# Kernel optimization log

Measured on AMD Instinct MI355X. Metric: run time of the kernel, lower is better.

The kernel has to match this reference:

```python
import jax, jax.numpy as jnp
import numpy as np

B, H, W = 8192, 5, 5
DICT, SE, CC, E, NZ = 14, 32, 64, 256, 512
EPS = 1e-4


def _conv(x, w, b):
    # x: [B,C,H,W], w: [O,C,3,3] -> SAME padding, stride 1
    y = jax.lax.conv_general_dilated(x, w, (1, 1), 'SAME',
                                     dimension_numbers=('NCHW', 'OIHW', 'NCHW'))
    return y + b[None, :, None, None]


def _embed(idx, table, cw, cb):
    emb = table[idx]                                  # [B,H,W,SE]
    # nn.Embedding(max_norm=1): renorm looked-up rows to norm <= 1
    n = jnp.sqrt(jnp.sum(emb * emb, axis=-1, keepdims=True))
    emb = emb * jnp.minimum(1.0, 1.0 / (n + 1e-7))
    x = jnp.transpose(emb, (0, 3, 1, 2))              # [B,SE,H,W]
    return _conv(x, cw, cb)                           # [B,CC,H,W]


def _phi(x, w1, b1, w2, b2, lw, lb):
    x = jax.nn.relu(_conv(x, w1, b1))
    x = jax.nn.relu(_conv(x, w2, b2))
    x = x.reshape(x.shape[0], -1)                     # [B, 32*H*W]
    x = x @ lw.T + lb                                 # [B, E]
    return x / (jnp.sqrt(jnp.sum(x * x, axis=1, keepdims=True)) + EPS)


def setup_inputs() -> dict:
    key = jax.random.key(0)
    ks = jax.random.split(key, 20)
    g = lambda k, s, sc=0.05: (jax.random.normal(k, s, jnp.float32) * sc)
    return {
        's': jax.random.randint(ks[0], (B, H, W), 0, DICT, dtype=jnp.int32),
        's_prime': jax.random.randint(ks[1], (B, H, W), 0, DICT, dtype=jnp.int32),
        'embed_table': g(ks[2], (DICT, SE), 1.0),
        'conv_embed_w': g(ks[3], (CC, SE, 3, 3)),
        'conv_embed_b': g(ks[4], (CC,)),
        'phi1_conv1_w': g(ks[5], (16, CC, 3, 3)),
        'phi1_conv1_b': g(ks[6], (16,)),
        'phi1_conv2_w': g(ks[7], (32, 16, 3, 3)),
        'phi1_conv2_b': g(ks[8], (32,)),
        'phi1_lin_w': g(ks[9], (E, H * W * 32)),
        'phi1_lin_b': g(ks[10], (E,)),
        'phi2_conv1_w': g(ks[11], (16, CC, 3, 3)),
        'phi2_conv1_b': g(ks[12], (16,)),
        'phi2_conv2_w': g(ks[13], (32, 16, 3, 3)),
        'phi2_conv2_b': g(ks[14], (32,)),
        'phi2_lin_w': g(ks[15], (E, H * W * 32)),
        'phi2_lin_b': g(ks[16], (E,)),
        'z_vectors': g(ks[17], (NZ, E), 1.0),
        'scale': jnp.ones((1,), jnp.float32),
    }


def reference(s, s_prime, embed_table, conv_embed_w, conv_embed_b,
              phi1_conv1_w, phi1_conv1_b, phi1_conv2_w, phi1_conv2_b,
              phi1_lin_w, phi1_lin_b,
              phi2_conv1_w, phi2_conv1_b, phi2_conv2_w, phi2_conv2_b,
              phi2_lin_w, phi2_lin_b, z_vectors, scale):
    xs = _embed(s, embed_table, conv_embed_w, conv_embed_b)
    xsp = _embed(s_prime, embed_table, conv_embed_w, conv_embed_b)
    embed1 = _phi(xs, phi1_conv1_w, phi1_conv1_b, phi1_conv2_w, phi1_conv2_b,
                  phi1_lin_w, phi1_lin_b)                 # [B,E]
    embed2 = _phi(xsp - xs, phi2_conv1_w, phi2_conv1_b, phi2_conv2_w,
                  phi2_conv2_b, phi2_lin_w, phi2_lin_b)   # [B,E]
    # codebook: L2-normalize (eps=0), cosine argmax, gather
    zn = z_vectors / jnp.sqrt(jnp.sum(z_vectors * z_vectors, axis=1, keepdims=True))
    z_inds = jnp.argmax(embed2 @ zn.T, axis=1)            # [B]
    z_matrix = zn[z_inds]                                 # [B,E]
    gramm = embed1 @ z_matrix.T                           # [B,B]
    return jnp.exp(scale) * gramm
```

## Files before the change

kernel.cpp:

```cpp
#include <hip/hip_runtime.h>
#include <hip/hip_bf16.h>

#define NB    8192
#define DICT  14
#define SE    32
#define CC    64
#define EDIM  256
#define NZV   512
#define C1N   16
#define C2N   32
#define J400  400
#define K800  800

typedef __attribute__((ext_vector_type(8))) short bf16x8;
typedef __attribute__((ext_vector_type(4))) float f32x4;

__device__ __forceinline__ void split_hl(float x, unsigned short& h, unsigned short& l) {
    unsigned u = __float_as_uint(x);
    unsigned short hh = (unsigned short)(u >> 16);
    float hf = __uint_as_float((unsigned)hh << 16);
    float lof = x - hf;
    unsigned ul = __float_as_uint(lof);
    l = (unsigned short)((ul + 0x7FFFu + ((ul >> 16) & 1u)) >> 16);
    h = hh;
}

__global__ __launch_bounds__(64) void k_norm_embed(const float* __restrict__ tab,
                                                   float* __restrict__ tn) {
    int d = blockIdx.x, l = threadIdx.x;
    float v = (l < SE) ? tab[d * SE + l] : 0.f;
    float s = v * v;
    #pragma unroll
    for (int o = 32; o > 0; o >>= 1) s += __shfl_down(s, o, 64);
    s = __shfl(s, 0, 64);
    float sc = fminf(1.f, 1.f / (sqrtf(s) + 1e-7f));
    if (l < SE) tn[d * SE + l] = v * sc;
}

__global__ __launch_bounds__(256) void k_norm_z(const float* __restrict__ z,
                                                unsigned short* __restrict__ znh,
                                                unsigned short* __restrict__ znl) {
    __shared__ float red[4];
    int r = blockIdx.x, t = threadIdx.x;
    float v = z[r * EDIM + t];
    float s = v * v;
    #pragma unroll
    for (int o = 32; o > 0; o >>= 1) s += __shfl_down(s, o, 64);
    if ((t & 63) == 0) red[t >> 6] = s;
    __syncthreads();
    float tot = red[0] + red[1] + red[2] + red[3];
    float nv = v / sqrtf(tot);
    unsigned short h, l;
    split_hl(nv, h, l);
    znh[r * EDIM + t] = h;
    znl[r * EDIM + t] = l;
}

__global__ __launch_bounds__(256) void k_prep_w(const float* __restrict__ lwa,
                                                const float* __restrict__ lwb,
                                                unsigned short* __restrict__ wh,
                                                unsigned short* __restrict__ wl) {
    int i = blockIdx.x * 256 + threadIdx.x;
    const int tot = 2 * EDIM * K800;
    if (i >= tot) return;
    float v = (i < EDIM * K800) ? lwa[i] : lwb[i - EDIM * K800];
    unsigned short h, l;
    split_hl(v, h, l);
    wh[i] = h; wl[i] = l;
}

__global__ __launch_bounds__(256) void k_build_A(const float* __restrict__ we,
                                                 const float* __restrict__ tn,
                                                 float* __restrict__ A) {
    int i = blockIdx.x * 256 + threadIdx.x;
    if (i >= DICT * CC * 9) return;
    int f = i % 9, c1 = (i / 9) % CC, d = i / (9 * CC);
    float acc = 0.f;
    #pragma unroll
    for (int c0 = 0; c0 < SE; c0++) acc += we[(c1 * SE + c0) * 9 + f] * tn[d * SE + c0];
    A[i] = acc;
}

__global__ __launch_bounds__(256) void k_build_beff(const float* __restrict__ w1a,
                                                    const float* __restrict__ b1a,
                                                    const float* __restrict__ w1b,
                                                    const float* __restrict__ b1b,
                                                    const float* __restrict__ be,
                                                    float* __restrict__ beff) {
    int t = blockIdx.x;
    const float* w1 = t ? w1b : w1a;
    const float* b1 = t ? b1b : b1a;
    for (int j = threadIdx.x; j < J400; j += blockDim.x) {
        int o = j / 25, y = (j / 5) % 5, x = j % 5;
        float acc = b1[o];
        if (t == 0) {
            for (int ey = 0; ey < 3; ey++) {
                int py = y + ey - 1; if (py < 0 || py > 4) continue;
                for (int ex = 0; ex < 3; ex++) {
                    int px = x + ex - 1; if (px < 0 || px > 4) continue;
                    for (int c1 = 0; c1 < CC; c1++)
                        acc += w1[((o * CC + c1) * 3 + ey) * 3 + ex] * be[c1];
                }
            }
        }
        beff[t * J400 + j] = acc;
    }
}

__global__ __launch_bounds__(256) void k_build_T(const float* __restrict__ w1a,
                                                 const float* __restrict__ w1b,
                                                 const float* __restrict__ A,
                                                 float* __restrict__ T) {
    int t = blockIdx.y;
    int qd = blockIdx.x;
    int d = qd % DICT, q = qd / DICT;
    int qy = q / 5, qx = q % 5;
    const float* w1 = t ? w1b : w1a;
    __shared__ float w1s[C1N * CC * 9];
    __shared__ float As[CC * 9];
    for (int i = threadIdx.x; i < C1N * CC * 9; i += 256) w1s[i] = w1[i];
    for (int i = threadIdx.x; i < CC * 9; i += 256) As[i] = A[d * CC * 9 + i];
    __syncthreads();
    float* Tout = T + (((size_t)t * 25 + q) * DICT + d) * J400;
    for (int j = threadIdx.x; j < J400; j += 256) {
        int o = j / 25, y = (j / 5) % 5, x = j % 5;
        float acc = 0.f;
        int py0 = max(0, max(y - 1, qy - 1)), py1 = min(4, min(y + 1, qy + 1));
        int px0 = max(0, max(x - 1, qx - 1)), px1 = min(4, min(x + 1, qx + 1));
        for (int py = py0; py <= py1; py++)
            for (int px = px0; px <= px1; px++) {
                int ey = py - y + 1, ex = px - x + 1;
                int fy = qy - py + 1, fx = qx - px + 1;
                const float* wp = &w1s[(o * CC) * 9 + (ey * 3 + ex)];
                const float* ap = &As[fy * 3 + fx];
                float pa = 0.f;
                #pragma unroll 8
                for (int c1 = 0; c1 < CC; c1++) pa += wp[c1 * 9] * ap[c1 * 9];
                acc += pa;
            }
        Tout[j] = acc;
    }
}

__global__ __launch_bounds__(256) void k_stage1(const int* __restrict__ s,
                                                const int* __restrict__ sp,
                                                const float* __restrict__ T,
                                                const float* __restrict__ beff,
                                                float* __restrict__ a1f) {
    int phi = blockIdx.y;
    __shared__ int s_sh[32][25], sp_sh[32][25];
    __shared__ float a_sh[32][J400 + 1];
    int b0 = blockIdx.x * 32;
    for (int i = threadIdx.x; i < 32 * 25; i += 256) {
        int si = i / 25, q = i % 25;
        s_sh[si][q] = s[(b0 + si) * 25 + q];
        if (phi) sp_sh[si][q] = sp[(b0 + si) * 25 + q];
    }
    __syncthreads();
    const float* Tt = T + (size_t)phi * 25 * DICT * J400;
    const float* be = beff + phi * J400;
    if (phi == 0) {
        for (int task = threadIdx.x; task < 32 * J400; task += 256) {
            int j = task % J400, si = task / J400;
            float acc = be[j];
            #pragma unroll
            for (int q = 0; q < 25; q++)
                acc += Tt[(q * DICT + s_sh[si][q]) * J400 + j];
            a_sh[si][j] = fmaxf(acc, 0.f);
        }
    } else {
        for (int task = threadIdx.x; task < 32 * J400; task += 256) {
            int j = task % J400, si = task / J400;
            float acc = be[j];
            #pragma unroll
            for (int q = 0; q < 25; q++)
                acc += Tt[(q * DICT + sp_sh[si][q]) * J400 + j]
                     - Tt[(q * DICT + s_sh[si][q]) * J400 + j];
            a_sh[si][j] = fmaxf(acc, 0.f);
        }
    }
    __syncthreads();
    float* outp = a1f + (size_t)phi * J400 * NB;
    for (int i = threadIdx.x; i < 32 * J400; i += 256) {
        int bl = i % 32, j = i / 32;
        outp[(size_t)j * NB + b0 + bl] = a_sh[bl][j];
    }
}

__global__ __launch_bounds__(256) void k_conv2(const float* __restrict__ a1f,
                                               const float* __restrict__ w2a,
                                               const float* __restrict__ b2a,
                                               const float* __restrict__ w2b,
                                               const float* __restrict__ b2b,
                                               float* __restrict__ a2f) {
    int t = blockIdx.y;
    const float* w2  = t ? w2b : w2a;
    const float* b2  = t ? b2b : b2a;
    const float* in0 = a1f + (size_t)t * J400 * NB;
    float* out0      = a2f + (size_t)t * K800 * NB;
    int b  = blockIdx.x * 64 + (threadIdx.x & 63);
    int og = blockIdx.z * 4 + (threadIdx.x >> 6);
    for (int o2g = 0; o2g < 4; o2g++) {
        int o2 = og * 4 + o2g;
        float acc[25];
        float bias = b2[o2];
        #pragma unroll
        for (int p = 0; p < 25; p++) acc[p] = bias;
        for (int c1 = 0; c1 < C1N; c1++) {
            float in[25];
            #pragma unroll
            for (int p = 0; p < 25; p++) in[p] = in0[(size_t)(c1 * 25 + p) * NB + b];
            #pragma unroll
            for (int ky = 0; ky < 3; ky++)
            #pragma unroll
            for (int kx = 0; kx < 3; kx++) {
                float w = w2[((o2 * C1N + c1) * 3 + ky) * 3 + kx];
                #pragma unroll
                for (int y = 0; y < 5; y++) {
                    int iy = y + ky - 1; if (iy < 0 || iy > 4) continue;
                    #pragma unroll
                    for (int x = 0; x < 5; x++) {
                        int ix = x + kx - 1; if (ix < 0 || ix > 4) continue;
                        acc[y * 5 + x] += w * in[iy * 5 + ix];
                    }
                }
            }
        }
        #pragma unroll
        for (int p = 0; p < 25; p++)
            out0[(size_t)(o2 * 25 + p) * NB + b] = fmaxf(acc[p], 0.f);
    }
}

__global__ __launch_bounds__(256) void k_linear_mfma(const float* __restrict__ a2f,
        const unsigned short* __restrict__ wh, const unsigned short* __restrict__ wl,
        const float* __restrict__ lba, const float* __restrict__ lbb,
        unsigned short* __restrict__ eh, unsigned short* __restrict__ el) {
    int phi = blockIdx.y;
    const float* Am = a2f + (size_t)phi * K800 * NB;
    const unsigned short* Wh = wh + (size_t)phi * EDIM * K800;
    const unsigned short* Wl = wl + (size_t)phi * EDIM * K800;
    const float* bias = phi ? lbb : lba;
    int b0 = blockIdx.x * 32;
    int tid = threadIdx.x;
    int wv = tid >> 6, lane = tid & 63, li = lane & 15, quad = lane >> 4;
    int n0 = wv * 64;
    int sb = tid & 31, kc = (tid >> 5) * 4;
    __shared__ __align__(16) unsigned short AhS[32][40], AlS[32][40];
    __shared__ float red[32][4];
    f32x4 acc[2][4];
    f32x4 zz = {0.f, 0.f, 0.f, 0.f};
    #pragma unroll
    for (int i = 0; i < 2; i++)
        #pragma unroll
        for (int j = 0; j < 4; j++) acc[i][j] = zz;

    for (int k0 = 0; k0 < K800; k0 += 32) {
        float x0 = Am[(size_t)(k0 + kc + 0) * NB + b0 + sb];
        float x1 = Am[(size_t)(k0 + kc + 1) * NB + b0 + sb];
        float x2 = Am[(size_t)(k0 + kc + 2) * NB + b0 + sb];
        float x3 = Am[(size_t)(k0 + kc + 3) * NB + b0 + sb];
        __syncthreads();
        unsigned short h0, l0, h1, l1, h2, l2, h3, l3;
        split_hl(x0, h0, l0); split_hl(x1, h1, l1);
        split_hl(x2, h2, l2); split_hl(x3, h3, l3);
        *(ushort4*)&AhS[sb][kc] = make_ushort4(h0, h1, h2, h3);
        *(ushort4*)&AlS[sb][kc] = make_ushort4(l0, l1, l2, l3);
        __syncthreads();
        bf16x8 ah0 = *(const bf16x8*)&AhS[li][quad * 8];
        bf16x8 ah1 = *(const bf16x8*)&AhS[16 + li][quad * 8];
        bf16x8 al0 = *(const bf16x8*)&AlS[li][quad * 8];
        bf16x8 al1 = *(const bf16x8*)&AlS[16 + li][quad * 8];
        #pragma unroll
        for (int nt = 0; nt < 4; nt++) {
            size_t wo = (size_t)(n0 + nt * 16 + li) * K800 + k0 + quad * 8;
            bf16x8 bh = *(const bf16x8*)(Wh + wo);
            bf16x8 bl = *(const bf16x8*)(Wl + wo);
            acc[0][nt] = __builtin_amdgcn_mfma_f32_16x16x32_bf16(ah0, bh, acc[0][nt], 0, 0, 0);
            acc[0][nt] = __builtin_amdgcn_mfma_f32_16x16x32_bf16(ah0, bl, acc[0][nt], 0, 0, 0);
            acc[0][nt] = __builtin_amdgcn_mfma_f32_16x16x32_bf16(al0, bh, acc[0][nt], 0, 0, 0);
            acc[1][nt] = __builtin_amdgcn_mfma_f32_16x16x32_bf16(ah1, bh, acc[1][nt], 0, 0, 0);
            acc[1][nt] = __builtin_amdgcn_mfma_f32_16x16x32_bf16(ah1, bl, acc[1][nt], 0, 0, 0);
            acc[1][nt] = __builtin_amdgcn_mfma_f32_16x16x32_bf16(al1, bh, acc[1][nt], 0, 0, 0);
        }
    }
    float q[2][4];
    #pragma unroll
    for (int mt = 0; mt < 2; mt++)
        #pragma unroll
        for (int r = 0; r < 4; r++) q[mt][r] = 0.f;
    #pragma unroll
    for (int mt = 0; mt < 2; mt++)
        #pragma unroll
        for (int nt = 0; nt < 4; nt++) {
            float bsv = bias[n0 + nt * 16 + li];
            #pragma unroll
            for (int r = 0; r < 4; r++) {
                float v = acc[mt][nt][r] + bsv;
                acc[mt][nt][r] = v;
                q[mt][r] += v * v;
            }
        }
    #pragma unroll
    for (int off = 1; off < 16; off <<= 1) {
        #pragma unroll
        for (int mt = 0; mt < 2; mt++)
            #pragma unroll
            for (int r = 0; r < 4; r++)
                q[mt][r] += __shfl_xor(q[mt][r], off, 64);
    }
    if (li == 0) {
        #pragma unroll
        for (int mt = 0; mt < 2; mt++)
            #pragma unroll
            for (int r = 0; r < 4; r++)
                red[mt * 16 + quad * 4 + r][wv] = q[mt][r];
    }
    __syncthreads();
    #pragma unroll
    for (int mt = 0; mt < 2; mt++) {
        #pragma unroll
        for (int r = 0; r < 4; r++) {
            int row = mt * 16 + quad * 4 + r;
            float tot = red[row][0] + red[row][1] + red[row][2] + red[row][3];
            float inv = 1.f / (sqrtf(tot) + 1e-4f);
            size_t base = (size_t)(phi * NB + b0 + row) * EDIM;
            #pragma unroll
            for (int nt = 0; nt < 4; nt++) {
                float v = acc[mt][nt][r] * inv;
                unsigned short h, l;
                split_hl(v, h, l);
                eh[base + n0 + nt * 16 + li] = h;
                el[base + n0 + nt * 16 + li] = l;
            }
        }
    }
}

__global__ __launch_bounds__(256) void k_scores_mfma(const unsigned short* __restrict__ eh,
        const unsigned short* __restrict__ el,
        const unsigned short* __restrict__ znh, const unsigned short* __restrict__ znl,
        float* __restrict__ C) {
    int m0 = blockIdx.x * 64;
    int wv = threadIdx.x >> 6, lane = threadIdx.x & 63;
    int li = lane & 15, quad = lane >> 4;
    int n0 = blockIdx.y * 256 + wv * 64;
    f32x4 acc[4][4];
    f32x4 zz = {0.f, 0.f, 0.f, 0.f};
    #pragma unroll
    for (int i = 0; i < 4; i++)
        #pragma unroll
        for (int j = 0; j < 4; j++) acc[i][j] = zz;
    for (int k0 = 0; k0 < EDIM; k0 += 32) {
        bf16x8 ah[4], al[4];
        #pragma unroll
        for (int mt = 0; mt < 4; mt++) {
            size_t ao = (size_t)(m0 + mt * 16 + li) * EDIM + k0 + quad * 8;
            ah[mt] = *(const bf16x8*)(eh + ao);
            al[mt] = *(const bf16x8*)(el + ao);
        }
        #pragma unroll
        for (int nt = 0; nt < 4; nt++) {
            size_t bo = (size_t)(n0 + nt * 16 + li) * EDIM + k0 + quad * 8;
            bf16x8 bh = *(const bf16x8*)(znh + bo);
            bf16x8 bl = *(const bf16x8*)(znl + bo);
            #pragma unroll
            for (int mt = 0; mt < 4; mt++) {
                acc[mt][nt] = __builtin_amdgcn_mfma_f32_16x16x32_bf16(ah[mt], bh, acc[mt][nt], 0, 0, 0);
                acc[mt][nt] = __builtin_amdgcn_mfma_f32_16x16x32_bf16(ah[mt], bl, acc[mt][nt], 0, 0, 0);
                acc[mt][nt] = __builtin_amdgcn_mfma_f32_16x16x32_bf16(al[mt], bh, acc[mt][nt], 0, 0, 0);
            }
        }
    }
    #pragma unroll
    for (int mt = 0; mt < 4; mt++)
        #pragma unroll
        for (int nt = 0; nt < 4; nt++)
            #pragma unroll
            for (int r = 0; r < 4; r++)
                C[(size_t)(m0 + mt * 16 + quad * 4 + r) * NZV + n0 + nt * 16 + li] = acc[mt][nt][r];
}

__global__ __launch_bounds__(64) void k_argmax(const float* __restrict__ C,
                                               int* __restrict__ idx) {
    int b = blockIdx.x, l = threadIdx.x;
    const float* row = C + (size_t)(NB + b) * NZV;
    float best = -3.0e38f; int bi = 0;
    for (int n = l; n < NZV; n += 64) {
        float v = row[n];
        if (v > best) { best = v; bi = n; }
    }
    #pragma unroll
    for (int o = 32; o > 0; o >>= 1) {
        float ov = __shfl_down(best, o, 64);
        int   oi = __shfl_down(bi, o, 64);
        if (ov > best || (ov == best && oi < bi)) { best = ov; bi = oi; }
    }
    if (l == 0) idx[b] = bi;
}

__global__ __launch_bounds__(256) void k_out(const float* __restrict__ C,
                                             const int* __restrict__ idx,
                                             const float* __restrict__ scale,
                                             float* __restrict__ out) {
    __shared__ float g[8][NZV];
    __shared__ int   id[2048];
    int i0 = blockIdx.y * 8;
    int j0 = blockIdx.x * 2048;
    float esc = expf(scale[0]);
    for (int u = threadIdx.x; u < 2048; u += 256) id[u] = idx[j0 + u];
    for (int u = threadIdx.x; u < 8 * NZV; u += 256) {
        int r = u >> 9, c = u & 511;
        g[r][c] = C[(size_t)(i0 + r) * NZV + c];
    }
    __syncthreads();
    int jb = threadIdx.x * 8;
    int myid[8];
    #pragma unroll
    for (int u = 0; u < 8; u++) myid[u] = id[jb + u];
    #pragma unroll
    for (int r = 0; r < 8; r++) {
        float4 o0, o1;
        o0.x = esc * g[r][myid[0]]; o0.y = esc * g[r][myid[1]];
        o0.z = esc * g[r][myid[2]]; o0.w = esc * g[r][myid[3]];
        o1.x = esc * g[r][myid[4]]; o1.y = esc * g[r][myid[5]];
        o1.z = esc * g[r][myid[6]]; o1.w = esc * g[r][myid[7]];
        float4* dst = (float4*)(out + (size_t)(i0 + r) * NB + j0 + jb);
        dst[0] = o0; dst[1] = o1;
    }
}

extern "C" void kernel_launch(void* const* d_in, const int* in_sizes, int n_in,
                              void* d_out, int out_size, void* d_ws, size_t ws_size,
                              hipStream_t stream) {
    const int*   s     = (const int*)d_in[0];
    const int*   sp    = (const int*)d_in[1];
    const float* tab   = (const float*)d_in[2];
    const float* wE    = (const float*)d_in[3];
    const float* bE    = (const float*)d_in[4];
    const float* w1a   = (const float*)d_in[5];
    const float* b1a   = (const float*)d_in[6];
    const float* w2a   = (const float*)d_in[7];
    const float* b2a   = (const float*)d_in[8];
    const float* lwa   = (const float*)d_in[9];
    const float* lba   = (const float*)d_in[10];
    const float* w1b   = (const float*)d_in[11];
    const float* b1b   = (const float*)d_in[12];
    const float* w2b   = (const float*)d_in[13];
    const float* b2b   = (const float*)d_in[14];
    const float* lwb   = (const float*)d_in[15];
    const float* lbb   = (const float*)d_in[16];
    const float* zv    = (const float*)d_in[17];
    const float* scale = (const float*)d_in[18];

    float* out = (float*)d_out;
    float* wsf = (float*)d_ws;

    float* tn   = wsf;
    float* Aw   = wsf + 448;
    float* beff = wsf + 8512;
    int*   idx  = (int*)(wsf + 9312);
    float* T    = wsf + 17504;
    float* Cm   = wsf + 297504;
    unsigned short* znh = (unsigned short*)(wsf + 8686112);
    unsigned short* znl = (unsigned short*)(wsf + 8751648);
    unsigned short* wh  = (unsigned short*)(wsf + 8817184);
    unsigned short* wl  = (unsigned short*)(wsf + 9021984);
    unsigned short* eh  = (unsigned short*)(wsf + 9226784);
    unsigned short* el  = (unsigned short*)(wsf + 11323936);

    float* a1f = out;
    float* a2f = out + 6553600;

    k_norm_embed<<<DICT, 64, 0, stream>>>(tab, tn);
    k_norm_z<<<NZV, 256, 0, stream>>>(zv, znh, znl);
    k_prep_w<<<1600, 256, 0, stream>>>(lwa, lwb, wh, wl);
    k_build_A<<<32, 256, 0, stream>>>(wE, tn, Aw);
    k_build_beff<<<2, 256, 0, stream>>>(w1a, b1a, w1b, b1b, bE, beff);
    k_build_T<<<dim3(25 * DICT, 2), 256, 0, stream>>>(w1a, w1b, Aw, T);
    k_stage1<<<dim3(NB / 32, 2), 256, 0, stream>>>(s, sp, T, beff, a1f);
    k_conv2<<<dim3(NB / 64, 2, 2), 256, 0, stream>>>(a1f, w2a, b2a, w2b, b2b, a2f);
    k_linear_mfma<<<dim3(NB / 32, 2), 256, 0, stream>>>(a2f, wh, wl, lba, lbb, eh, el);
    k_scores_mfma<<<dim3(2 * NB / 64, NZV / 256), 256, 0, stream>>>(eh, el, znh, znl, Cm);
    k_argmax<<<NB, 64, 0, stream>>>(Cm, idx);
    k_out<<<dim3(NB / 2048, NB / 8), 256, 0, stream>>>(Cm, idx, scale, out);
}
```

Baseline: 609.9 us.

## Fuse stage1, conv2, linear, scores and argmax into one per-tile kernel

Merges the table-lookup first conv, second conv, split-bf16 MFMA linear layer, normalization, codebook scoring and argmax into a single kernel that keeps each 32-sample tile in LDS. The large a1/a2/embedding intermediates no longer round-trip through global memory. The small prep kernels are also merged to cut launches. The fused kernel uses about 78 KB of LDS, which limits occupancy, and the conv2 stage now runs per tile with syncs between output-channel chunks.

```diff
diff --git a/kernel.cpp b/kernel.cpp
--- a/kernel.cpp
+++ b/kernel.cpp
@@ -9,8 +9,6 @@
 #define NZV   512
 #define C1N   16
 #define C2N   32
-#define J400  400
-#define K800  800
 
 typedef __attribute__((ext_vector_type(8))) short bf16x8;
 typedef __attribute__((ext_vector_type(4))) float f32x4;
@@ -37,73 +35,69 @@
     if (l < SE) tn[d * SE + l] = v * sc;
 }
 
-__global__ __launch_bounds__(256) void k_norm_z(const float* __restrict__ z,
-                                                unsigned short* __restrict__ znh,
-                                                unsigned short* __restrict__ znl) {
-    __shared__ float red[4];
-    int r = blockIdx.x, t = threadIdx.x;
-    float v = z[r * EDIM + t];
-    float s = v * v;
-    #pragma unroll
-    for (int o = 32; o > 0; o >>= 1) s += __shfl_down(s, o, 64);
-    if ((t & 63) == 0) red[t >> 6] = s;
-    __syncthreads();
-    float tot = red[0] + red[1] + red[2] + red[3];
-    float nv = v / sqrtf(tot);
-    unsigned short h, l;
-    split_hl(nv, h, l);
-    znh[r * EDIM + t] = h;
-    znl[r * EDIM + t] = l;
-}
-
-__global__ __launch_bounds__(256) void k_prep_w(const float* __restrict__ lwa,
-                                                const float* __restrict__ lwb,
-                                                unsigned short* __restrict__ wh,
-                                                unsigned short* __restrict__ wl) {
-    int i = blockIdx.x * 256 + threadIdx.x;
-    const int tot = 2 * EDIM * K800;
-    if (i >= tot) return;
-    float v = (i < EDIM * K800) ? lwa[i] : lwb[i - EDIM * K800];
-    unsigned short h, l;
-    split_hl(v, h, l);
-    wh[i] = h; wl[i] = l;
-}
-
-__global__ __launch_bounds__(256) void k_build_A(const float* __restrict__ we,
-                                                 const float* __restrict__ tn,
-                                                 float* __restrict__ A) {
-    int i = blockIdx.x * 256 + threadIdx.x;
-    if (i >= DICT * CC * 9) return;
-    int f = i % 9, c1 = (i / 9) % CC, d = i / (9 * CC);
-    float acc = 0.f;
-    #pragma unroll
-    for (int c0 = 0; c0 < SE; c0++) acc += we[(c1 * SE + c0) * 9 + f] * tn[d * SE + c0];
-    A[i] = acc;
-}
-
-__global__ __launch_bounds__(256) void k_build_beff(const float* __restrict__ w1a,
-                                                    const float* __restrict__ b1a,
-                                                    const float* __restrict__ w1b,
-                                                    const float* __restrict__ b1b,
-                                                    const float* __restrict__ be,
-                                                    float* __restrict__ beff) {
-    int t = blockIdx.x;
-    const float* w1 = t ? w1b : w1a;
-    const float* b1 = t ? b1b : b1a;
-    for (int j = threadIdx.x; j < J400; j += blockDim.x) {
-        int o = j / 25, y = (j / 5) % 5, x = j % 5;
-        float acc = b1[o];
-        if (t == 0) {
-            for (int ey = 0; ey < 3; ey++) {
-                int py = y + ey - 1; if (py < 0 || py > 4) continue;
-                for (int ex = 0; ex < 3; ex++) {
-                    int px = x + ex - 1; if (px < 0 || px > 4) continue;
-                    for (int c1 = 0; c1 < CC; c1++)
-                        acc += w1[((o * CC + c1) * 3 + ey) * 3 + ex] * be[c1];
-                }
-            }
-        }
-        beff[t * J400 + j] = acc;
+__global__ __launch_bounds__(256) void k_prep_zw(const float* __restrict__ z,
+        const float* __restrict__ lwa, const float* __restrict__ lwb,
+        unsigned short* __restrict__ znh, unsigned short* __restrict__ znl,
+        unsigned short* __restrict__ wh, unsigned short* __restrict__ wl) {
+    int bid = blockIdx.x, t = threadIdx.x;
+    if (bid < NZV) {
+        __shared__ float red[4];
+        float v = z[bid * EDIM + t];
+        float s = v * v;
+        #pragma unroll
+        for (int o = 32; o > 0; o >>= 1) s += __shfl_down(s, o, 64);
+        if ((t & 63) == 0) red[t >> 6] = s;
+        __syncthreads();
+        float tot = red[0] + red[1] + red[2] + red[3];
+        float nv = v / sqrtf(tot);
+        unsigned short h, l;
+        split_hl(nv, h, l);
+        znh[bid * EDIM + t] = h;
+        znl[bid * EDIM + t] = l;
+    } else {
+        int i = (bid - NZV) * 256 + t;
+        if (i < 2 * EDIM * 800) {
+            float v = (i < EDIM * 800) ? lwa[i] : lwb[i - EDIM * 800];
+            unsigned short h, l;
+            split_hl(v, h, l);
+            wh[i] = h; wl[i] = l;
+        }
+    }
+}
+
+__global__ __launch_bounds__(256) void k_prep_ab(const float* __restrict__ we,
+        const float* __restrict__ tn,
+        const float* __restrict__ w1a, const float* __restrict__ b1a,
+        const float* __restrict__ w1b, const float* __restrict__ b1b,
+        const float* __restrict__ be,
+        float* __restrict__ A, float* __restrict__ beff) {
+    if (blockIdx.x < 32) {
+        int i = blockIdx.x * 256 + threadIdx.x;
+        if (i >= DICT * CC * 9) return;
+        int f = i % 9, c1 = (i / 9) % CC, d = i / (9 * CC);
+        float acc = 0.f;
+        #pragma unroll
+        for (int c0 = 0; c0 < SE; c0++) acc += we[(c1 * SE + c0) * 9 + f] * tn[d * SE + c0];
+        A[i] = acc;
+    } else {
+        int t = blockIdx.x - 32;
+        const float* w1 = t ? w1b : w1a;
+        const float* b1 = t ? b1b : b1a;
+        for (int j = threadIdx.x; j < 400; j += blockDim.x) {
+            int o = j / 25, y = (j / 5) % 5, x = j % 5;
+            float acc = b1[o];
+            if (t == 0) {
+                for (int ey = 0; ey < 3; ey++) {
+                    int py = y + ey - 1; if (py < 0 || py > 4) continue;
+                    for (int ex = 0; ex < 3; ex++) {
+                        int px = x + ex - 1; if (px < 0 || px > 4) continue;
+                        for (int c1 = 0; c1 < CC; c1++)
+                            acc += w1[((o * CC + c1) * 3 + ey) * 3 + ex] * be[c1];
+                    }
+                }
+            }
+            beff[t * 400 + j] = acc;
+        }
     }
 }
 
@@ -121,8 +115,8 @@
     for (int i = threadIdx.x; i < C1N * CC * 9; i += 256) w1s[i] = w1[i];
     for (int i = threadIdx.x; i < CC * 9; i += 256) As[i] = A[d * CC * 9 + i];
     __syncthreads();
-    float* Tout = T + (((size_t)t * 25 + q) * DICT + d) * J400;
-    for (int j = threadIdx.x; j < J400; j += 256) {
+    float* Tout = T + (((size_t)t * 25 + q) * DICT + d) * 400;
+    for (int j = threadIdx.x; j < 400; j += 256) {
         int o = j / 25, y = (j / 5) % 5, x = j % 5;
         float acc = 0.f;
         int py0 = max(0, max(y - 1, qy - 1)), py1 = min(4, min(y + 1, qy + 1));
@@ -142,74 +136,88 @@
     }
 }
 
-__global__ __launch_bounds__(256) void k_stage1(const int* __restrict__ s,
-                                                const int* __restrict__ sp,
-                                                const float* __restrict__ T,
-                                                const float* __restrict__ beff,
-                                                float* __restrict__ a1f) {
+__global__ __launch_bounds__(256, 2) void k_phi(
+    const int* __restrict__ s, const int* __restrict__ sp,
+    const float* __restrict__ T, const float* __restrict__ beff,
+    const float* __restrict__ w2a, const float* __restrict__ b2a,
+    const float* __restrict__ w2b, const float* __restrict__ b2b,
+    const unsigned short* __restrict__ wh, const unsigned short* __restrict__ wl,
+    const float* __restrict__ lba, const float* __restrict__ lbb,
+    const unsigned short* __restrict__ znh, const unsigned short* __restrict__ znl,
+    float* __restrict__ Cm, int* __restrict__ idxout) {
     int phi = blockIdx.y;
-    __shared__ int s_sh[32][25], sp_sh[32][25];
-    __shared__ float a_sh[32][J400 + 1];
     int b0 = blockIdx.x * 32;
-    for (int i = threadIdx.x; i < 32 * 25; i += 256) {
-        int si = i / 25, q = i % 25;
-        s_sh[si][q] = s[(b0 + si) * 25 + q];
-        if (phi) sp_sh[si][q] = sp[(b0 + si) * 25 + q];
-    }
-    __syncthreads();
-    const float* Tt = T + (size_t)phi * 25 * DICT * J400;
-    const float* be = beff + phi * J400;
+    int tid = threadIdx.x;
+    int wv = tid >> 6, lane = tid & 63, li = lane & 15, quad = lane >> 4;
+
+    __shared__ __align__(16) char smem[79936];
+    float* a1T          = (float*)smem;
+    unsigned short* a2h = (unsigned short*)(smem + 52800);
+    unsigned short* a2l = (unsigned short*)(smem + 65600);
+    int* sbase1         = (int*)(smem + 52800);
+    int* sbase2         = (int*)(smem + 56000);
+    float* redq         = (float*)(smem + 78400);
+    float* argv         = (float*)(smem + 78912);
+    int*   argn         = (int*)(smem + 79424);
+    unsigned short* emh = (unsigned short*)smem;
+    unsigned short* eml = (unsigned short*)(smem + 16896);
+
+    const float* Tg = T + (size_t)phi * (25 * DICT * 400);
+
+    for (int i = tid; i < 800; i += 256) {
+        int si = i / 25, q = i - si * 25;
+        sbase1[i] = (q * DICT + s[(b0 + si) * 25 + q]) * 400;
+        if (phi) sbase2[i] = (q * DICT + sp[(b0 + si) * 25 + q]) * 400;
+    }
+    __syncthreads();
+
+    const float* be = beff + phi * 400;
     if (phi == 0) {
-        for (int task = threadIdx.x; task < 32 * J400; task += 256) {
-            int j = task % J400, si = task / J400;
+        for (int task = tid; task < 12800; task += 256) {
+            int si = task / 400, j = task - si * 400;
             float acc = be[j];
-            #pragma unroll
-            for (int q = 0; q < 25; q++)
-                acc += Tt[(q * DICT + s_sh[si][q]) * J400 + j];
-            a_sh[si][j] = fmaxf(acc, 0.f);
+            const int* sb = sbase1 + si * 25;
+            #pragma unroll
+            for (int q = 0; q < 25; q++) acc += Tg[sb[q] + j];
+            a1T[j * 33 + si] = fmaxf(acc, 0.f);
         }
     } else {
-        for (int task = threadIdx.x; task < 32 * J400; task += 256) {
-            int j = task % J400, si = task / J400;
+        for (int task = tid; task < 12800; task += 256) {
+            int si = task / 400, j = task - si * 400;
             float acc = be[j];
-            #pragma unroll
-            for (int q = 0; q < 25; q++)
-                acc += Tt[(q * DICT + sp_sh[si][q]) * J400 + j]
-                     - Tt[(q * DICT + s_sh[si][q]) * J400 + j];
-            a_sh[si][j] = fmaxf(acc, 0.f);
-        }
-    }
-    __syncthreads();
-    float* outp = a1f + (size_t)phi * J400 * NB;
-    for (int i = threadIdx.x; i < 32 * J400; i += 256) {
-        int bl = i % 32, j = i / 32;
-        outp[(size_t)j * NB + b0 + bl] = a_sh[bl][j];
-    }
-}
-
-__global__ __launch_bounds__(256) void k_conv2(const float* __restrict__ a1f,
-                                               const float* __restrict__ w2a,
-                                               const float* __restrict__ b2a,
-                                               const float* __restrict__ w2b,
-                                               const float* __restrict__ b2b,
-                                               float* __restrict__ a2f) {
-    int t = blockIdx.y;
-    const float* w2  = t ? w2b : w2a;
-    const float* b2  = t ? b2b : b2a;
-    const float* in0 = a1f + (size_t)t * J400 * NB;
-    float* out0      = a2f + (size_t)t * K800 * NB;
-    int b  = blockIdx.x * 64 + (threadIdx.x & 63);
-    int og = blockIdx.z * 4 + (threadIdx.x >> 6);
-    for (int o2g = 0; o2g < 4; o2g++) {
-        int o2 = og * 4 + o2g;
-        float acc[25];
-        float bias = b2[o2];
-        #pragma unroll
-        for (int p = 0; p < 25; p++) acc[p] = bias;
+            const int* sb1 = sbase1 + si * 25;
+            const int* sb2 = sbase2 + si * 25;
+            #pragma unroll
+            for (int q = 0; q < 25; q++) acc += Tg[sb2[q] + j] - Tg[sb1[q] + j];
+            a1T[j * 33 + si] = fmaxf(acc, 0.f);
+        }
+    }
+    __syncthreads();
+
+    const float* w2 = phi ? w2b : w2a;
+    const float* b2 = phi ? b2b : b2a;
+    const unsigned short* Wh = wh + (size_t)phi * EDIM * 800;
+    const unsigned short* Wl = wl + (size_t)phi * EDIM * 800;
+    int n0w = wv * 64;
+    f32x4 acc2[2][4];
+    f32x4 zz = {0.f, 0.f, 0.f, 0.f};
+    #pragma unroll
+    for (int i = 0; i < 2; i++)
+        #pragma unroll
+        for (int j = 0; j < 4; j++) acc2[i][j] = zz;
+    bf16x8 zfrag = {0, 0, 0, 0, 0, 0, 0, 0};
+
+    int csi = tid >> 3, o2loc = tid & 7;
+    for (int c = 0; c < 4; c++) {
+        int o2 = c * 8 + o2loc;
+        float cacc[25];
+        float bias2 = b2[o2];
+        #pragma unroll
+        for (int p = 0; p < 25; p++) cacc[p] = bias2;
         for (int c1 = 0; c1 < C1N; c1++) {
-            float in[25];
-            #pragma unroll
-            for (int p = 0; p < 25; p++) in[p] = in0[(size_t)(c1 * 25 + p) * NB + b];
+            float row[25];
+            #pragma unroll
+            for (int p = 0; p < 25; p++) row[p] = a1T[(c1 * 25 + p) * 33 + csi];
             #pragma unroll
             for (int ky = 0; ky < 3; ky++)
             #pragma unroll
@@ -221,182 +229,179 @@
                     #pragma unroll
                     for (int x = 0; x < 5; x++) {
                         int ix = x + kx - 1; if (ix < 0 || ix > 4) continue;
-                        acc[y * 5 + x] += w * in[iy * 5 + ix];
+                        cacc[y * 5 + x] += w * row[iy * 5 + ix];
                     }
                 }
             }
         }
         #pragma unroll
-        for (int p = 0; p < 25; p++)
-            out0[(size_t)(o2 * 25 + p) * NB + b] = fmaxf(acc[p], 0.f);
-    }
-}
-
-__global__ __launch_bounds__(256) void k_linear_mfma(const float* __restrict__ a2f,
-        const unsigned short* __restrict__ wh, const unsigned short* __restrict__ wl,
-        const float* __restrict__ lba, const float* __restrict__ lbb,
-        unsigned short* __restrict__ eh, unsigned short* __restrict__ el) {
-    int phi = blockIdx.y;
-    const float* Am = a2f + (size_t)phi * K800 * NB;
-    const unsigned short* Wh = wh + (size_t)phi * EDIM * K800;
-    const unsigned short* Wl = wl + (size_t)phi * EDIM * K800;
-    const float* bias = phi ? lbb : lba;
-    int b0 = blockIdx.x * 32;
-    int tid = threadIdx.x;
-    int wv = tid >> 6, lane = tid & 63, li = lane & 15, quad = lane >> 4;
-    int n0 = wv * 64;
-    int sb = tid & 31, kc = (tid >> 5) * 4;
-    __shared__ __align__(16) unsigned short AhS[32][40], AlS[32][40];
-    __shared__ float red[32][4];
-    f32x4 acc[2][4];
-    f32x4 zz = {0.f, 0.f, 0.f, 0.f};
-    #pragma unroll
-    for (int i = 0; i < 2; i++)
-        #pragma unroll
-        for (int j = 0; j < 4; j++) acc[i][j] = zz;
-
-    for (int k0 = 0; k0 < K800; k0 += 32) {
-        float x0 = Am[(size_t)(k0 + kc + 0) * NB + b0 + sb];
-        float x1 = Am[(size_t)(k0 + kc + 1) * NB + b0 + sb];
-        float x2 = Am[(size_t)(k0 + kc + 2) * NB + b0 + sb];
-        float x3 = Am[(size_t)(k0 + kc + 3) * NB + b0 + sb];
+        for (int p = 0; p < 25; p++) {
+            float v = fmaxf(cacc[p], 0.f);
+            unsigned short h, l;
+            split_hl(v, h, l);
+            int ko = csi * 200 + o2loc * 25 + p;
+            a2h[ko] = h; a2l[ko] = l;
+        }
         __syncthreads();
-        unsigned short h0, l0, h1, l1, h2, l2, h3, l3;
-        split_hl(x0, h0, l0); split_hl(x1, h1, l1);
-        split_hl(x2, h2, l2); split_hl(x3, h3, l3);
-        *(ushort4*)&AhS[sb][kc] = make_ushort4(h0, h1, h2, h3);
-        *(ushort4*)&AlS[sb][kc] = make_ushort4(l0, l1, l2, l3);
+        #pragma unroll
+        for (int ks = 0; ks < 7; ks++) {
+            bf16x8 ah0, al0, ah1, al1;
+            if (ks < 6) {
+                int ko = ks * 32 + quad * 8;
+                ah0 = *(const bf16x8*)&a2h[li * 200 + ko];
+                al0 = *(const bf16x8*)&a2l[li * 200 + ko];
+                ah1 = *(const bf16x8*)&a2h[(16 + li) * 200 + ko];
+                al1 = *(const bf16x8*)&a2l[(16 + li) * 200 + ko];
+            } else {
+                ah0 = zfrag; al0 = zfrag; ah1 = zfrag; al1 = zfrag;
+                if (quad == 0) {
+                    ah0 = *(const bf16x8*)&a2h[li * 200 + 192];
+                    al0 = *(const bf16x8*)&a2l[li * 200 + 192];
+                    ah1 = *(const bf16x8*)&a2h[(16 + li) * 200 + 192];
+                    al1 = *(const bf16x8*)&a2l[(16 + li) * 200 + 192];
+                }
+            }
+            int kglob = c * 200 + ks * 32 + quad * 8;
+            #pragma unroll
+            for (int nt = 0; nt < 4; nt++) {
+                size_t wo = (size_t)(n0w + nt * 16 + li) * 800 + kglob;
+                bf16x8 bh = *(const bf16x8*)(Wh + wo);
+                bf16x8 bl = *(const bf16x8*)(Wl + wo);
+                acc2[0][nt] = __builtin_amdgcn_mfma_f32_16x16x32_bf16(ah0, bh, acc2[0][nt], 0, 0, 0);
+                acc2[0][nt] = __builtin_amdgcn_mfma_f32_16x16x32_bf16(ah0, bl, acc2[0][nt], 0, 0, 0);
+                acc2[0][nt] = __builtin_amdgcn_mfma_f32_16x16x32_bf16(al0, bh, acc2[0][nt], 0, 0, 0);
+                acc2[1][nt] = __builtin_amdgcn_mfma_f32_16x16x32_bf16(ah1, bh, acc2[1][nt], 0, 0, 0);
+                acc2[1][nt] = __builtin_amdgcn_mfma_f32_16x16x32_bf16(ah1, bl, acc2[1][nt], 0, 0, 0);
+                acc2[1][nt] = __builtin_amdgcn_mfma_f32_16x16x32_bf16(al1, bh, acc2[1][nt], 0, 0, 0);
+            }
+        }
         __syncthreads();
-        bf16x8 ah0 = *(const bf16x8*)&AhS[li][quad * 8];
-        bf16x8 ah1 = *(const bf16x8*)&AhS[16 + li][quad * 8];
-        bf16x8 al0 = *(const bf16x8*)&AlS[li][quad * 8];
-        bf16x8 al1 = *(const bf16x8*)&AlS[16 + li][quad * 8];
+    }
+
+    const float* lb = phi ? lbb : lba;
+    float sq[2][4];
+    #pragma unroll
+    for (int mt = 0; mt < 2; mt++)
+        #pragma unroll
+        for (int r = 0; r < 4; r++) sq[mt][r] = 0.f;
+    #pragma unroll
+    for (int mt = 0; mt < 2; mt++)
         #pragma unroll
         for (int nt = 0; nt < 4; nt++) {
-            size_t wo = (size_t)(n0 + nt * 16 + li) * K800 + k0 + quad * 8;
-            bf16x8 bh = *(const bf16x8*)(Wh + wo);
-            bf16x8 bl = *(const bf16x8*)(Wl + wo);
-            acc[0][nt] = __builtin_amdgcn_mfma_f32_16x16x32_bf16(ah0, bh, acc[0][nt], 0, 0, 0);
-            acc[0][nt] = __builtin_amdgcn_mfma_f32_16x16x32_bf16(ah0, bl, acc[0][nt], 0, 0, 0);
-            acc[0][nt] = __builtin_amdgcn_mfma_f32_16x16x32_bf16(al0, bh, acc[0][nt], 0, 0, 0);
-            acc[1][nt] = __builtin_amdgcn_mfma_f32_16x16x32_bf16(ah1, bh, acc[1][nt], 0, 0, 0);
-            acc[1][nt] = __builtin_amdgcn_mfma_f32_16x16x32_bf16(ah1, bl, acc[1][nt], 0, 0, 0);
-            acc[1][nt] = __builtin_amdgcn_mfma_f32_16x16x32_bf16(al1, bh, acc[1][nt], 0, 0, 0);
-        }
-    }
-    float q[2][4];
+            float bsv = lb[n0w + nt * 16 + li];
+            #pragma unroll
+            for (int r = 0; r < 4; r++) {
+                float v = acc2[mt][nt][r] + bsv;
+                acc2[mt][nt][r] = v;
+                sq[mt][r] += v * v;
+            }
+        }
+    #pragma unroll
+    for (int off = 1; off < 16; off <<= 1)
+        #pragma unroll
+        for (int mt = 0; mt < 2; mt++)
+            #pragma unroll
+            for (int r = 0; r < 4; r++)
+                sq[mt][r] += __shfl_xor(sq[mt][r], off, 64);
+    if (li == 0) {
+        #pragma unroll
+        for (int mt = 0; mt < 2; mt++)
+            #pragma unroll
+            for (int r = 0; r < 4; r++)
+                redq[(mt * 16 + quad * 4 + r) * 4 + wv] = sq[mt][r];
+    }
+    __syncthreads();
     #pragma unroll
     for (int mt = 0; mt < 2; mt++)
         #pragma unroll
-        for (int r = 0; r < 4; r++) q[mt][r] = 0.f;
-    #pragma unroll
-    for (int mt = 0; mt < 2; mt++)
-        #pragma unroll
-        for (int nt = 0; nt < 4; nt++) {
-            float bsv = bias[n0 + nt * 16 + li];
-            #pragma unroll
-            for (int r = 0; r < 4; r++) {
-                float v = acc[mt][nt][r] + bsv;
-                acc[mt][nt][r] = v;
-                q[mt][r] += v * v;
-            }
-        }
-    #pragma unroll
-    for (int off = 1; off < 16; off <<= 1) {
-        #pragma unroll
-        for (int mt = 0; mt < 2; mt++)
-            #pragma unroll
-            for (int r = 0; r < 4; r++)
-                q[mt][r] += __shfl_xor(q[mt][r], off, 64);
-    }
-    if (li == 0) {
-        #pragma unroll
-        for (int mt = 0; mt < 2; mt++)
-            #pragma unroll
-            for (int r = 0; r < 4; r++)
-                red[mt * 16 + quad * 4 + r][wv] = q[mt][r];
-    }
-    __syncthreads();
-    #pragma unroll
-    for (int mt = 0; mt < 2; mt++) {
-        #pragma unroll
         for (int r = 0; r < 4; r++) {
-            int row = mt * 16 + quad * 4 + r;
-            float tot = red[row][0] + red[row][1] + red[row][2] + red[row][3];
+            int rowm = mt * 16 + quad * 4 + r;
+            float tot = redq[rowm * 4 + 0] + redq[rowm * 4 + 1] +
+                        redq[rowm * 4 + 2] + redq[rowm * 4 + 3];
             float inv = 1.f / (sqrtf(tot) + 1e-4f);
-            size_t base = (size_t)(phi * NB + b0 + row) * EDIM;
             #pragma unroll
             for (int nt = 0; nt < 4; nt++) {
-                float v = acc[mt][nt][r] * inv;
+                float v = acc2[mt][nt][r] * inv;
                 unsigned short h, l;
                 split_hl(v, h, l);
-                eh[base + n0 + nt * 16 + li] = h;
-                el[base + n0 + nt * 16 + li] = l;
-            }
-        }
-    }
-}
-
-__global__ __launch_bounds__(256) void k_scores_mfma(const unsigned short* __restrict__ eh,
-        const unsigned short* __restrict__ el,
-        const unsigned short* __restrict__ znh, const unsigned short* __restrict__ znl,
-        float* __restrict__ C) {
-    int m0 = blockIdx.x * 64;
-    int wv = threadIdx.x >> 6, lane = threadIdx.x & 63;
-    int li = lane & 15, quad = lane >> 4;
-    int n0 = blockIdx.y * 256 + wv * 64;
-    f32x4 acc[4][4];
-    f32x4 zz = {0.f, 0.f, 0.f, 0.f};
-    #pragma unroll
-    for (int i = 0; i < 4; i++)
-        #pragma unroll
-        for (int j = 0; j < 4; j++) acc[i][j] = zz;
-    for (int k0 = 0; k0 < EDIM; k0 += 32) {
-        bf16x8 ah[4], al[4];
-        #pragma unroll
-        for (int mt = 0; mt < 4; mt++) {
-            size_t ao = (size_t)(m0 + mt * 16 + li) * EDIM + k0 + quad * 8;
-            ah[mt] = *(const bf16x8*)(eh + ao);
-            al[mt] = *(const bf16x8*)(el + ao);
-        }
-        #pragma unroll
-        for (int nt = 0; nt < 4; nt++) {
-            size_t bo = (size_t)(n0 + nt * 16 + li) * EDIM + k0 + quad * 8;
-            bf16x8 bh = *(const bf16x8*)(znh + bo);
-            bf16x8 bl = *(const bf16x8*)(znl + bo);
-            #pragma unroll
-            for (int mt = 0; mt < 4; mt++) {
-                acc[mt][nt] = __builtin_amdgcn_mfma_f32_16x16x32_bf16(ah[mt], bh, acc[mt][nt], 0, 0, 0);
-                acc[mt][nt] = __builtin_amdgcn_mfma_f32_16x16x32_bf16(ah[mt], bl, acc[mt][nt], 0, 0, 0);
-                acc[mt][nt] = __builtin_amdgcn_mfma_f32_16x16x32_bf16(al[mt], bh, acc[mt][nt], 0, 0, 0);
-            }
-        }
-    }
-    #pragma unroll
-    for (int mt = 0; mt < 4; mt++)
-        #pragma unroll
-        for (int nt = 0; nt < 4; nt++)
-            #pragma unroll
-            for (int r = 0; r < 4; r++)
-                C[(size_t)(m0 + mt * 16 + quad * 4 + r) * NZV + n0 + nt * 16 + li] = acc[mt][nt][r];
-}
-
-__global__ __launch_bounds__(64) void k_argmax(const float* __restrict__ C,
-                                               int* __restrict__ idx) {
-    int b = blockIdx.x, l = threadIdx.x;
-    const float* row = C + (size_t)(NB + b) * NZV;
-    float best = -3.0e38f; int bi = 0;
-    for (int n = l; n < NZV; n += 64) {
-        float v = row[n];
-        if (v > best) { best = v; bi = n; }
-    }
-    #pragma unroll
-    for (int o = 32; o > 0; o >>= 1) {
-        float ov = __shfl_down(best, o, 64);
-        int   oi = __shfl_down(bi, o, 64);
-        if (ov > best || (ov == best && oi < bi)) { best = ov; bi = oi; }
-    }
-    if (l == 0) idx[b] = bi;
+                int col = n0w + nt * 16 + li;
+                emh[rowm * 264 + col] = h;
+                eml[rowm * 264 + col] = l;
+            }
+        }
+    __syncthreads();
+
+    f32x4 acc3[2][8];
+    #pragma unroll
+    for (int i = 0; i < 2; i++)
+        #pragma unroll
+        for (int j = 0; j < 8; j++) acc3[i][j] = zz;
+    int zn0 = wv * 128;
+    #pragma unroll
+    for (int ks = 0; ks < 8; ks++) {
+        int ko = ks * 32 + quad * 8;
+        bf16x8 ah0 = *(const bf16x8*)&emh[li * 264 + ko];
+        bf16x8 al0 = *(const bf16x8*)&eml[li * 264 + ko];
+        bf16x8 ah1 = *(const bf16x8*)&emh[(16 + li) * 264 + ko];
+        bf16x8 al1 = *(const bf16x8*)&eml[(16 + li) * 264 + ko];
+        #pragma unroll
+        for (int nt = 0; nt < 8; nt++) {
+            size_t zo = (size_t)(zn0 + nt * 16 + li) * EDIM + ko;
+            bf16x8 bh = *(const bf16x8*)(znh + zo);
+            bf16x8 bl = *(const bf16x8*)(znl + zo);
+            acc3[0][nt] = __builtin_amdgcn_mfma_f32_16x16x32_bf16(ah0, bh, acc3[0][nt], 0, 0, 0);
+            acc3[0][nt] = __builtin_amdgcn_mfma_f32_16x16x32_bf16(ah0, bl, acc3[0][nt], 0, 0, 0);
+            acc3[0][nt] = __builtin_amdgcn_mfma_f32_16x16x32_bf16(al0, bh, acc3[0][nt], 0, 0, 0);
+            acc3[1][nt] = __builtin_amdgcn_mfma_f32_16x16x32_bf16(ah1, bh, acc3[1][nt], 0, 0, 0);
+            acc3[1][nt] = __builtin_amdgcn_mfma_f32_16x16x32_bf16(ah1, bl, acc3[1][nt], 0, 0, 0);
+            acc3[1][nt] = __builtin_amdgcn_mfma_f32_16x16x32_bf16(al1, bh, acc3[1][nt], 0, 0, 0);
+        }
+    }
+
+    if (phi == 0) {
+        #pragma unroll
+        for (int mt = 0; mt < 2; mt++)
+            #pragma unroll
+            for (int nt = 0; nt < 8; nt++)
+                #pragma unroll
+                for (int r = 0; r < 4; r++)
+                    Cm[(size_t)(b0 + mt * 16 + quad * 4 + r) * NZV + zn0 + nt * 16 + li] =
+                        acc3[mt][nt][r];
+    } else {
+        #pragma unroll
+        for (int mt = 0; mt < 2; mt++)
+            #pragma unroll
+            for (int r = 0; r < 4; r++) {
+                float best = -3.0e38f; int bn = 0;
+                #pragma unroll
+                for (int nt = 0; nt < 8; nt++) {
+                    float v = acc3[mt][nt][r];
+                    int n = zn0 + nt * 16 + li;
+                    if (v > best) { best = v; bn = n; }
+                }
+                #pragma unroll
+                for (int off = 1; off < 16; off <<= 1) {
+                    float ov = __shfl_xor(best, off, 64);
+                    int   on = __shfl_xor(bn, off, 64);
+                    if (ov > best || (ov == best && on < bn)) { best = ov; bn = on; }
+                }
+                if (li == 0) {
+                    int rowm = mt * 16 + quad * 4 + r;
+                    argv[rowm * 4 + wv] = best;
+                    argn[rowm * 4 + wv] = bn;
+                }
+            }
+        __syncthreads();
+        if (tid < 32) {
+            float best = argv[tid * 4]; int bn = argn[tid * 4];
+            #pragma unroll
+            for (int w = 1; w < 4; w++) {
+                float v = argv[tid * 4 + w]; int n = argn[tid * 4 + w];
+                if (v > best || (v == best && n < bn)) { best = v; bn = n; }
+            }
+            idxout[b0 + tid] = bn;
+        }
+    }
 }
 
 __global__ __launch_bounds__(256) void k_out(const float* __restrict__ C,
@@ -462,26 +467,16 @@
     int*   idx  = (int*)(wsf + 9312);
     float* T    = wsf + 17504;
     float* Cm   = wsf + 297504;
-    unsigned short* znh = (unsigned short*)(wsf + 8686112);
-    unsigned short* znl = (unsigned short*)(wsf + 8751648);
-    unsigned short* wh  = (unsigned short*)(wsf + 8817184);
-    unsigned short* wl  = (unsigned short*)(wsf + 9021984);
-    unsigned short* eh  = (unsigned short*)(wsf + 9226784);
-    unsigned short* el  = (unsigned short*)(wsf + 11323936);
-
-    float* a1f = out;
-    float* a2f = out + 6553600;
+    unsigned short* wh  = (unsigned short*)(wsf + 4491808);
+    unsigned short* wl  = (unsigned short*)(wsf + 4696608);
+    unsigned short* znh = (unsigned short*)(wsf + 4901408);
+    unsigned short* znl = (unsigned short*)(wsf + 4966944);
 
     k_norm_embed<<<DICT, 64, 0, stream>>>(tab, tn);
-    k_norm_z<<<NZV, 256, 0, stream>>>(zv, znh, znl);
-    k_prep_w<<<1600, 256, 0, stream>>>(lwa, lwb, wh, wl);
-    k_build_A<<<32, 256, 0, stream>>>(wE, tn, Aw);
-    k_build_beff<<<2, 256, 0, stream>>>(w1a, b1a, w1b, b1b, bE, beff);
+    k_prep_zw<<<NZV + 1600, 256, 0, stream>>>(zv, lwa, lwb, znh, znl, wh, wl);
+    k_prep_ab<<<34, 256, 0, stream>>>(wE, tn, w1a, b1a, w1b, b1b, bE, Aw, beff);
     k_build_T<<<dim3(25 * DICT, 2), 256, 0, stream>>>(w1a, w1b, Aw, T);
-    k_stage1<<<dim3(NB / 32, 2), 256, 0, stream>>>(s, sp, T, beff, a1f);
-    k_conv2<<<dim3(NB / 64, 2, 2), 256, 0, stream>>>(a1f, w2a, b2a, w2b, b2b, a2f);
-    k_linear_mfma<<<dim3(NB / 32, 2), 256, 0, stream>>>(a2f, wh, wl, lba, lbb, eh, el);
-    k_scores_mfma<<<dim3(2 * NB / 64, NZV / 256), 256, 0, stream>>>(eh, el, znh, znl, Cm);
-    k_argmax<<<NB, 64, 0, stream>>>(Cm, idx);
+    k_phi<<<dim3(NB / 32, 2), 256, 0, stream>>>(s, sp, T, beff, w2a, b2a, w2b, b2b,
+                                                wh, wl, lba, lbb, znh, znl, Cm, idx);
     k_out<<<dim3(NB / 2048, NB / 8), 256, 0, stream>>>(Cm, idx, scale, out);
 }
```

Result: faster. 531.0 us (-12.9%).
